# Performance work log

Hardware: AMD Instinct MI355X
Metric: run time of the kernel (lower is better)

The kernel has to match this reference:

```python
import jax, jax.numpy as jnp
import numpy as np

N_NODES = 50000
N_GRAPHS = 512
EPS = 1e-5


def _ln(x, g, b):
    mu = jnp.mean(x, axis=-1, keepdims=True)
    var = jnp.var(x, axis=-1, keepdims=True)
    return (x - mu) * jax.lax.rsqrt(var + EPS) * g + b


def _sage(x, src, dst, wl, wr, bl):
    # mean-aggregate neighbor features: messages x[src] -> dst
    s = jax.ops.segment_sum(x[src], dst, num_segments=N_NODES)
    cnt = jax.ops.segment_sum(jnp.ones((src.shape[0],), x.dtype), dst, num_segments=N_NODES)
    agg = s / jnp.maximum(cnt, 1.0)[:, None]
    # PyG SAGEConv: lin_l(agg) + lin_r(x), bias only on lin_l
    return agg @ wl + bl + x @ wr


def setup_inputs() -> dict:
    key = jax.random.key(0)
    ks = jax.random.split(key, 16)
    C, H, NC, E = 128, 128, 2, 800000
    inp = {
        'x': jax.random.normal(ks[0], (N_NODES, C), jnp.float32),
        'edge_index': jax.random.randint(ks[1], (2, E), 0, N_NODES, jnp.int32),
        'batch': jnp.sort(jax.random.randint(ks[2], (N_NODES,), 0, N_GRAPHS, jnp.int32)),
    }
    def w(k, shape):
        return jax.random.normal(k, shape, jnp.float32) * 0.05
    inp.update({
        'w1l': w(ks[3], (C, H)), 'w1r': w(ks[4], (C, H)), 'b1': jnp.zeros((H,), jnp.float32),
        'g1': jnp.ones((H,), jnp.float32), 'be1': jnp.zeros((H,), jnp.float32),
        'w2l': w(ks[5], (H, H)), 'w2r': w(ks[6], (H, H)), 'b2': jnp.zeros((H,), jnp.float32),
        'g2': jnp.ones((H,), jnp.float32), 'be2': jnp.zeros((H,), jnp.float32),
        'w3l': w(ks[7], (H, H)), 'w3r': w(ks[8], (H, H)), 'b3': jnp.zeros((H,), jnp.float32),
        'g3': jnp.ones((H,), jnp.float32), 'be3': jnp.zeros((H,), jnp.float32),
        'wc': w(ks[9], (H, NC)), 'bc': jnp.zeros((NC,), jnp.float32),
    })
    return inp


def reference(x, edge_index, batch, w1l, w1r, b1, g1, be1, w2l, w2r, b2, g2, be2,
              w3l, w3r, b3, g3, be3, wc, bc):
    src, dst = edge_index[0], edge_index[1]
    # eval mode: dropout is identity
    h1 = _ln(jax.nn.relu(_sage(x, src, dst, w1l, w1r, b1)), g1, be1)
    h2 = _ln(jax.nn.relu(_sage(h1, src, dst, w2l, w2r, b2)) + h1, g2, be2)
    h3 = _ln(h2 + jax.nn.relu(_sage(h2, src, dst, w3l, w3r, b3)), g3, be3)
    # global mean pool over graphs
    s = jax.ops.segment_sum(h3, batch, num_segments=N_GRAPHS)
    cnt = jax.ops.segment_sum(jnp.ones((h3.shape[0],), h3.dtype), batch, num_segments=N_GRAPHS)
    avg = s / jnp.maximum(cnt, 1.0)[:, None]
    out = avg @ wc + bc
    return (out, h3, avg)
```

## Files before the change

kernel.cpp:

```cpp
#include <hip/hip_runtime.h>

#define NND 50000
#define NE  800000
#define CF  128
#define NGR 512
#define DCAP 64

typedef __bf16 bf16;
typedef __bf16 bf16x2 __attribute__((ext_vector_type(2)));
typedef __bf16 bf16x4 __attribute__((ext_vector_type(4)));
typedef __bf16 bf16x8 __attribute__((ext_vector_type(8)));
typedef float  f32x4  __attribute__((ext_vector_type(4)));

__device__ __forceinline__ int swz(int n, int k) {
  return n * 256 + (((k >> 3) ^ (n & 31)) << 3) + (k & 7);
}

__global__ __launch_bounds__(256) void conv_k(const float* __restrict__ x,
                                              bf16* __restrict__ xb,
                                              const float* __restrict__ w1l, const float* __restrict__ w1r,
                                              const float* __restrict__ w2l, const float* __restrict__ w2r,
                                              const float* __restrict__ w3l, const float* __restrict__ w3r,
                                              bf16* __restrict__ wb,
                                              const int* __restrict__ batch,
                                              int* __restrict__ gs,
                                              int* __restrict__ cnt) {
  int t = blockIdx.x * 256 + threadIdx.x;
  if (t < (NND * CF / 4)) {
    f32x4 v = ((const f32x4*)x)[t];
    bf16x4 o;
    o[0] = (bf16)v[0]; o[1] = (bf16)v[1]; o[2] = (bf16)v[2]; o[3] = (bf16)v[3];
    ((bf16x4*)xb)[t] = o;
  }
  if (t < 49152) {
    int m = t >> 13, w = t & 8191;
    const float* src = (m == 0) ? w1l : (m == 1) ? w1r : (m == 2) ? w2l
                     : (m == 3) ? w2r : (m == 4) ? w3l : w3r;
    float2 v = *(const float2*)(src + w * 2);
    bf16x2 o;
    o[0] = (bf16)v.x; o[1] = (bf16)v.y;
    ((bf16x2*)wb)[t] = o;
  }
  if (t < NND) {
    cnt[t] = 0;
    int b = batch[t];
    if (t == 0) {
      for (int g = 0; g <= b; g++) gs[g] = 0;
    } else {
      int pb = batch[t - 1];
      for (int g = pb + 1; g <= b; g++) gs[g] = t;
    }
    if (t == NND - 1) {
      for (int g = b + 1; g <= NGR; g++) gs[g] = NND;
    }
  }
}

__global__ __launch_bounds__(256) void fill_k(const int* __restrict__ src,
                                              const int* __restrict__ dst,
                                              int* __restrict__ cnt,
                                              unsigned short* __restrict__ csr) {
  int r  = blockIdx.x & 7;
  int lo = r * 6250, hi = lo + 6250;
  int base = (blockIdx.x >> 3) * 2048;
  int end  = min(base + 2048, NE);
  for (int e = base + threadIdx.x; e < end; e += 256) {
    int d = dst[e];
    if (d >= lo && d < hi) {
      int p = atomicAdd(&cnt[d], 1);
      if (p < DCAP) csr[d * DCAP + p] = (unsigned short)src[e];
    }
  }
}

__global__ __launch_bounds__(256) void agg_k(const bf16* __restrict__ xin,
                                             const int* __restrict__ cnt,
                                             const unsigned short* __restrict__ csr,
                                             bf16* __restrict__ aggout) {
  int wid  = (blockIdx.x * 256 + threadIdx.x) >> 6;
  int lane = threadIdx.x & 63;
  if (wid >= NND) return;
  int sub = lane >> 4;
  int c8  = (lane & 15) * 8;
  int deg = min(cnt[wid], DCAP);
  int ebase = wid * DCAP;
  float a[8] = {};
  for (int e = 0; e < deg; e += 16) {
    int   s[4];
    float m[4];
#pragma unroll
    for (int u = 0; u < 4; u++) {
      int i = e + u * 4 + sub;
      s[u] = csr[ebase + ((i < deg) ? i : 0)];
      m[u] = (i < deg) ? 1.f : 0.f;
    }
    bf16x8 v[4];
#pragma unroll
    for (int u = 0; u < 4; u++) v[u] = *(const bf16x8*)(xin + s[u] * 128 + c8);
#pragma unroll
    for (int u = 0; u < 4; u++)
#pragma unroll
      for (int j = 0; j < 8; j++) a[j] += m[u] * (float)v[u][j];
  }
#pragma unroll
  for (int j = 0; j < 8; j++) {
    a[j] += __shfl_xor(a[j], 16);
    a[j] += __shfl_xor(a[j], 32);
  }
  if (sub == 0) {
    float inv = 1.0f / fmaxf((float)deg, 1.0f);
    bf16x8 o;
#pragma unroll
    for (int j = 0; j < 8; j++) o[j] = (bf16)(a[j] * inv);
    *(bf16x8*)(aggout + wid * 128 + c8) = o;
  }
}

template <typename TO>
__global__ __launch_bounds__(256, 2) void gemm_k(
    const bf16* __restrict__ aggp, const bf16* __restrict__ prev,
    const bf16* __restrict__ wl, const bf16* __restrict__ wr,
    const float* __restrict__ bias, const float* __restrict__ gamma,
    const float* __restrict__ beta, TO* __restrict__ outp, int addres) {
  __shared__ bf16 bt[128 * 256];
  int tid = threadIdx.x;
  for (int e = tid; e < 128 * 64; e += 256) {
    int k  = e >> 6;
    int n2 = (e & 63) << 1;
    {
      bf16x2 v = *(const bf16x2*)(wl + k * 128 + n2);
      bt[swz(n2, k)]     = v[0];
      bt[swz(n2 + 1, k)] = v[1];
    }
    {
      bf16x2 v = *(const bf16x2*)(wr + k * 128 + n2);
      bt[swz(n2, k + 128)]     = v[0];
      bt[swz(n2 + 1, k + 128)] = v[1];
    }
  }
  __syncthreads();

  int wave = tid >> 6, lane = tid & 63;
  int q = lane >> 4, r = lane & 15;
  int wrow = blockIdx.x * 128 + wave * 32;

  int arow[2];
#pragma unroll
  for (int rt = 0; rt < 2; rt++) {
    int ar = wrow + rt * 16 + r;
    arow[rt] = (ar < NND) ? ar : (NND - 1);
  }

  f32x4 acc[2][8] = {};

#pragma unroll
  for (int kk = 0; kk < 8; kk++) {
    int kof = kk * 32 + q * 8;
    bf16x8 af[2];
#pragma unroll
    for (int rt = 0; rt < 2; rt++) {
      const bf16* ap = (kk < 4) ? (aggp + arow[rt] * 128 + kof)
                                : (prev + arow[rt] * 128 + (kof - 128));
      af[rt] = *(const bf16x8*)ap;
    }
#pragma unroll
    for (int t = 0; t < 8; t++) {
      int n = t * 16 + r;
      bf16x8 bfrag = *(const bf16x8*)&bt[n * 256 + (((kof >> 3) ^ (n & 31)) << 3)];
#pragma unroll
      for (int rt = 0; rt < 2; rt++)
        acc[rt][t] = __builtin_amdgcn_mfma_f32_16x16x32_bf16(af[rt], bfrag, acc[rt][t], 0, 0, 0);
    }
  }

  float biasf[8], gf[8], bef[8];
#pragma unroll
  for (int t = 0; t < 8; t++) {
    int c = t * 16 + r;
    biasf[t] = bias[c];
    gf[t]    = gamma[c];
    bef[t]   = beta[c];
  }

#pragma unroll
  for (int rt = 0; rt < 2; rt++) {
#pragma unroll
    for (int reg = 0; reg < 4; reg++) {
      int row = wrow + rt * 16 + q * 4 + reg;
      int rr  = (row < NND) ? row : (NND - 1);
      const bf16* prow = prev + rr * 128;
      float vals[8];
      float s = 0.f, s2 = 0.f;
#pragma unroll
      for (int t = 0; t < 8; t++) {
        float v = acc[rt][t][reg] + biasf[t];
        v = fmaxf(v, 0.f);
        if (addres) v += (float)prow[t * 16 + r];
        vals[t] = v;
        s += v;
        s2 += v * v;
      }
#pragma unroll
      for (int m = 1; m < 16; m <<= 1) {
        s  += __shfl_xor(s, m);
        s2 += __shfl_xor(s2, m);
      }
      float mean = s * (1.f / 128.f);
      float var  = fmaxf(s2 * (1.f / 128.f) - mean * mean, 0.f);
      float rstd = rsqrtf(var + 1e-5f);
      if (row < NND) {
        TO* orow = outp + row * 128;
#pragma unroll
        for (int t = 0; t < 8; t++)
          orow[t * 16 + r] = (TO)((vals[t] - mean) * rstd * gf[t] + bef[t]);
      }
    }
  }
}

__global__ __launch_bounds__(256) void poolhead_k(
    const float* __restrict__ h3, const int* __restrict__ gs,
    const float* __restrict__ wc, const float* __restrict__ bc,
    float* __restrict__ outv, float* __restrict__ avgv) {
  int g = blockIdx.x;
  int s = gs[g], epos = gs[g + 1];
  int tid = threadIdx.x;
  int wave = tid >> 6, lane = tid & 63;
  float a0 = 0.f, a1 = 0.f;
  for (int row = s + wave; row < epos; row += 4) {
    float2 v = *(const float2*)(h3 + row * 128 + 2 * lane);
    a0 += v.x; a1 += v.y;
  }
  __shared__ float red[4][128];
  red[wave][2 * lane]     = a0;
  red[wave][2 * lane + 1] = a1;
  __syncthreads();
  __shared__ float sp[4];
  if (tid < 128) {
    float t4  = red[0][tid] + red[1][tid] + red[2][tid] + red[3][tid];
    float inv = 1.f / fmaxf((float)(epos - s), 1.f);
    float avg = t4 * inv;
    avgv[g * 128 + tid] = avg;
    float p0 = avg * wc[tid * 2 + 0];
    float p1 = avg * wc[tid * 2 + 1];
#pragma unroll
    for (int m = 1; m < 64; m <<= 1) {
      p0 += __shfl_xor(p0, m);
      p1 += __shfl_xor(p1, m);
    }
    if ((tid & 63) == 0) {
      sp[(tid >> 6) * 2]     = p0;
      sp[(tid >> 6) * 2 + 1] = p1;
    }
  }
  __syncthreads();
  if (tid == 0) {
    outv[g * 2 + 0] = sp[0] + sp[2] + bc[0];
    outv[g * 2 + 1] = sp[1] + sp[3] + bc[1];
  }
}

extern "C" void kernel_launch(void* const* d_in, const int* in_sizes, int n_in,
                              void* d_out, int out_size, void* d_ws, size_t ws_size,
                              hipStream_t stream) {
  const float* x   = (const float*)d_in[0];
  const int* ei    = (const int*)d_in[1];
  const int* batch = (const int*)d_in[2];
  const float* w1l = (const float*)d_in[3],  *w1r = (const float*)d_in[4];
  const float* b1  = (const float*)d_in[5],  *g1  = (const float*)d_in[6],  *be1 = (const float*)d_in[7];
  const float* w2l = (const float*)d_in[8],  *w2r = (const float*)d_in[9];
  const float* b2  = (const float*)d_in[10], *g2  = (const float*)d_in[11], *be2 = (const float*)d_in[12];
  const float* w3l = (const float*)d_in[13], *w3r = (const float*)d_in[14];
  const float* b3  = (const float*)d_in[15], *g3  = (const float*)d_in[16], *be3 = (const float*)d_in[17];
  const float* wc  = (const float*)d_in[18], *bc  = (const float*)d_in[19];
  const int* srcv = ei;
  const int* dstv = ei + NE;

  char* base = (char*)d_ws;
  int*            cnt  = (int*)(base + 0);
  int*            gs   = (int*)(base + 200064);
  bf16*           wb   = (bf16*)(base + 202752);
  unsigned short* csr  = (unsigned short*)(base + 399360);
  bf16*           agg  = (bf16*)(base + 6799360);
  bf16*           h1   = (bf16*)(base + 19599360);
  bf16*           h2xb = (bf16*)(base + 32399360);

  bf16* wb1l = wb,          *wb1r = wb + 16384;
  bf16* wb2l = wb + 32768,  *wb2r = wb + 49152;
  bf16* wb3l = wb + 65536,  *wb3r = wb + 81920;

  float* outv = (float*)d_out;
  float* h3   = outv + 1024;
  float* avgv = outv + 1024 + NND * CF;

  conv_k<<<6250, 256, 0, stream>>>(x, h2xb, w1l, w1r, w2l, w2r, w3l, w3r, wb, batch, gs, cnt);
  fill_k<<<3128, 256, 0, stream>>>(srcv, dstv, cnt, csr);

  agg_k<<<12500, 256, 0, stream>>>(h2xb, cnt, csr, agg);
  gemm_k<bf16><<<391, 256, 0, stream>>>(agg, h2xb, wb1l, wb1r, b1, g1, be1, h1, 0);
  agg_k<<<12500, 256, 0, stream>>>(h1, cnt, csr, agg);
  gemm_k<bf16><<<391, 256, 0, stream>>>(agg, h1, wb2l, wb2r, b2, g2, be2, h2xb, 1);
  agg_k<<<12500, 256, 0, stream>>>(h2xb, cnt, csr, agg);
  gemm_k<float><<<391, 256, 0, stream>>>(agg, h2xb, wb3l, wb3r, b3, g3, be3, h3, 1);
  poolhead_k<<<NGR, 256, 0, stream>>>(h3, gs, wc, bc, outv, avgv);
}
```

Measured before the change: 315.4 us.

## Fuse neighbor mean aggregation into the SAGE GEMM kernel

Removes the separate aggregation kernel and its intermediate buffer. Each GEMM wave now gathers and averages its own rows' neighbor features from the CSR into registers, then feeds them straight into the MFMA A-fragments. This saves three kernel launches and the write and re-read of the aggregated activations. The cost is that the irregular gather now runs with far fewer threads (391 blocks instead of 12500), with each lane looping serially over the neighbors, so latency hiding may suffer.

```diff
diff --git a/kernel.cpp b/kernel.cpp
--- a/kernel.cpp
+++ b/kernel.cpp
@@ -73,52 +73,10 @@
   }
 }
 
-__global__ __launch_bounds__(256) void agg_k(const bf16* __restrict__ xin,
-                                             const int* __restrict__ cnt,
-                                             const unsigned short* __restrict__ csr,
-                                             bf16* __restrict__ aggout) {
-  int wid  = (blockIdx.x * 256 + threadIdx.x) >> 6;
-  int lane = threadIdx.x & 63;
-  if (wid >= NND) return;
-  int sub = lane >> 4;
-  int c8  = (lane & 15) * 8;
-  int deg = min(cnt[wid], DCAP);
-  int ebase = wid * DCAP;
-  float a[8] = {};
-  for (int e = 0; e < deg; e += 16) {
-    int   s[4];
-    float m[4];
-#pragma unroll
-    for (int u = 0; u < 4; u++) {
-      int i = e + u * 4 + sub;
-      s[u] = csr[ebase + ((i < deg) ? i : 0)];
-      m[u] = (i < deg) ? 1.f : 0.f;
-    }
-    bf16x8 v[4];
-#pragma unroll
-    for (int u = 0; u < 4; u++) v[u] = *(const bf16x8*)(xin + s[u] * 128 + c8);
-#pragma unroll
-    for (int u = 0; u < 4; u++)
-#pragma unroll
-      for (int j = 0; j < 8; j++) a[j] += m[u] * (float)v[u][j];
-  }
-#pragma unroll
-  for (int j = 0; j < 8; j++) {
-    a[j] += __shfl_xor(a[j], 16);
-    a[j] += __shfl_xor(a[j], 32);
-  }
-  if (sub == 0) {
-    float inv = 1.0f / fmaxf((float)deg, 1.0f);
-    bf16x8 o;
-#pragma unroll
-    for (int j = 0; j < 8; j++) o[j] = (bf16)(a[j] * inv);
-    *(bf16x8*)(aggout + wid * 128 + c8) = o;
-  }
-}
-
 template <typename TO>
-__global__ __launch_bounds__(256, 2) void gemm_k(
-    const bf16* __restrict__ aggp, const bf16* __restrict__ prev,
+__global__ __launch_bounds__(256, 2) void aggemm_k(
+    const bf16* __restrict__ xp,
+    const int* __restrict__ cnt, const unsigned short* __restrict__ csr,
     const bf16* __restrict__ wl, const bf16* __restrict__ wr,
     const float* __restrict__ bias, const float* __restrict__ gamma,
     const float* __restrict__ beta, TO* __restrict__ outp, int addres) {
@@ -151,17 +109,63 @@
     arow[rt] = (ar < NND) ? ar : (NND - 1);
   }
 
+  bf16x8 aggf[2][4];
+#pragma unroll
+  for (int rt = 0; rt < 2; rt++) {
+    int row = arow[rt];
+    int deg = min(cnt[row], DCAP);
+    const unsigned short* cp = csr + row * DCAP;
+    const bf16* xq = xp + q * 8;
+    float fa[4][8] = {};
+    int e = 0;
+    for (; e + 2 <= deg; e += 2) {
+      ushort2 ss = *(const ushort2*)(cp + e);
+      const bf16* p0 = xq + (int)ss.x * 128;
+      const bf16* p1 = xq + (int)ss.y * 128;
+      bf16x8 v0[4], v1[4];
+#pragma unroll
+      for (int kk = 0; kk < 4; kk++) {
+        v0[kk] = *(const bf16x8*)(p0 + kk * 32);
+        v1[kk] = *(const bf16x8*)(p1 + kk * 32);
+      }
+#pragma unroll
+      for (int kk = 0; kk < 4; kk++)
+#pragma unroll
+        for (int j = 0; j < 8; j++)
+          fa[kk][j] += (float)v0[kk][j] + (float)v1[kk][j];
+    }
+    if (e < deg) {
+      const bf16* p0 = xq + (int)cp[e] * 128;
+#pragma unroll
+      for (int kk = 0; kk < 4; kk++) {
+        bf16x8 vt = *(const bf16x8*)(p0 + kk * 32);
+#pragma unroll
+        for (int j = 0; j < 8; j++) fa[kk][j] += (float)vt[j];
+      }
+    }
+    float inv = 1.0f / fmaxf((float)deg, 1.0f);
+#pragma unroll
+    for (int kk = 0; kk < 4; kk++) {
+      bf16x8 o;
+#pragma unroll
+      for (int j = 0; j < 8; j++) o[j] = (bf16)(fa[kk][j] * inv);
+      aggf[rt][kk] = o;
+    }
+  }
+
   f32x4 acc[2][8] = {};
 
 #pragma unroll
   for (int kk = 0; kk < 8; kk++) {
     int kof = kk * 32 + q * 8;
     bf16x8 af[2];
-#pragma unroll
-    for (int rt = 0; rt < 2; rt++) {
-      const bf16* ap = (kk < 4) ? (aggp + arow[rt] * 128 + kof)
-                                : (prev + arow[rt] * 128 + (kof - 128));
-      af[rt] = *(const bf16x8*)ap;
+    if (kk < 4) {
+      af[0] = aggf[0][kk];
+      af[1] = aggf[1][kk];
+    } else {
+#pragma unroll
+      for (int rt = 0; rt < 2; rt++)
+        af[rt] = *(const bf16x8*)(xp + arow[rt] * 128 + (kof - 128));
     }
 #pragma unroll
     for (int t = 0; t < 8; t++) {
@@ -188,7 +192,7 @@
     for (int reg = 0; reg < 4; reg++) {
       int row = wrow + rt * 16 + q * 4 + reg;
       int rr  = (row < NND) ? row : (NND - 1);
-      const bf16* prow = prev + rr * 128;
+      const bf16* prow = xp + rr * 128;
       float vals[8];
       float s = 0.f, s2 = 0.f;
 #pragma unroll
@@ -281,7 +285,6 @@
   int*            gs   = (int*)(base + 200064);
   bf16*           wb   = (bf16*)(base + 202752);
   unsigned short* csr  = (unsigned short*)(base + 399360);
-  bf16*           agg  = (bf16*)(base + 6799360);
   bf16*           h1   = (bf16*)(base + 19599360);
   bf16*           h2xb = (bf16*)(base + 32399360);
 
@@ -296,11 +299,8 @@
   conv_k<<<6250, 256, 0, stream>>>(x, h2xb, w1l, w1r, w2l, w2r, w3l, w3r, wb, batch, gs, cnt);
   fill_k<<<3128, 256, 0, stream>>>(srcv, dstv, cnt, csr);
 
-  agg_k<<<12500, 256, 0, stream>>>(h2xb, cnt, csr, agg);
-  gemm_k<bf16><<<391, 256, 0, stream>>>(agg, h2xb, wb1l, wb1r, b1, g1, be1, h1, 0);
-  agg_k<<<12500, 256, 0, stream>>>(h1, cnt, csr, agg);
-  gemm_k<bf16><<<391, 256, 0, stream>>>(agg, h1, wb2l, wb2r, b2, g2, be2, h2xb, 1);
-  agg_k<<<12500, 256, 0, stream>>>(h2xb, cnt, csr, agg);
-  gemm_k<float><<<391, 256, 0, stream>>>(agg, h2xb, wb3l, wb3r, b3, g3, be3, h3, 1);
+  aggemm_k<bf16><<<391, 256, 0, stream>>>(h2xb, cnt, csr, wb1l, wb1r, b1, g1, be1, h1, 0);
+  aggemm_k<bf16><<<391, 256, 0, stream>>>(h1, cnt, csr, wb2l, wb2r, b2, g2, be2, h2xb, 1);
+  aggemm_k<float><<<391, 256, 0, stream>>>(h2xb, cnt, csr, wb3l, wb3r, b3, g3, be3, h3, 1);
   poolhead_k<<<NGR, 256, 0, stream>>>(h3, gs, wc, bc, outv, avgv);
 }
```

After: 349.9 us. 10.9% more time.

## Split aggregation across four column quarters and simplify CSR fill

Applied to the files above, without the earlier changes.

The edge-fill kernel drops its 8-way destination-range partitioning, in which each block rescanned its edge chunk and kept only one eighth of the destinations. Each thread now loads four edges with int4 loads and inserts all of them, so each edge is read once. The aggregation kernel now gives each wavefront one node and one 32-column quarter, with 16 edges gathered in parallel at 16 bytes per lane. That raises the grid to 50000 blocks and adds two extra shuffle steps. The trade is more parallelism and shorter per-wave gather chains against four times the CSR index reads and a less localised atomic pattern in the fill.

```diff
diff --git a/kernel.cpp b/kernel.cpp
--- a/kernel.cpp
+++ b/kernel.cpp
@@ -60,16 +60,17 @@
                                               const int* __restrict__ dst,
                                               int* __restrict__ cnt,
                                               unsigned short* __restrict__ csr) {
-  int r  = blockIdx.x & 7;
-  int lo = r * 6250, hi = lo + 6250;
-  int base = (blockIdx.x >> 3) * 2048;
-  int end  = min(base + 2048, NE);
-  for (int e = base + threadIdx.x; e < end; e += 256) {
-    int d = dst[e];
-    if (d >= lo && d < hi) {
-      int p = atomicAdd(&cnt[d], 1);
-      if (p < DCAP) csr[d * DCAP + p] = (unsigned short)src[e];
-    }
+  int e = blockIdx.x * 1024 + threadIdx.x * 4;
+  if (e >= NE) return;
+  int4 d4 = *(const int4*)(dst + e);
+  int4 s4 = *(const int4*)(src + e);
+  int dd[4] = {d4.x, d4.y, d4.z, d4.w};
+  int ss[4] = {s4.x, s4.y, s4.z, s4.w};
+#pragma unroll
+  for (int u = 0; u < 4; u++) {
+    int d = dd[u];
+    int p = atomicAdd(&cnt[d], 1);
+    if (p < DCAP) csr[d * DCAP + p] = (unsigned short)ss[u];
   }
 }
 
@@ -77,42 +78,57 @@
                                              const int* __restrict__ cnt,
                                              const unsigned short* __restrict__ csr,
                                              bf16* __restrict__ aggout) {
-  int wid  = (blockIdx.x * 256 + threadIdx.x) >> 6;
+  int b = blockIdx.x;
+  int q = b & 3;
+  int node = (b >> 2) * 4 + (threadIdx.x >> 6);
   int lane = threadIdx.x & 63;
-  if (wid >= NND) return;
-  int sub = lane >> 4;
-  int c8  = (lane & 15) * 8;
-  int deg = min(cnt[wid], DCAP);
-  int ebase = wid * DCAP;
+  int esub = lane >> 2;
+  int coff = q * 32 + (lane & 3) * 8;
+  int deg = min(cnt[node], DCAP);
+  int ebase = node * DCAP;
   float a[8] = {};
-  for (int e = 0; e < deg; e += 16) {
-    int   s[4];
-    float m[4];
-#pragma unroll
-    for (int u = 0; u < 4; u++) {
-      int i = e + u * 4 + sub;
-      s[u] = csr[ebase + ((i < deg) ? i : 0)];
-      m[u] = (i < deg) ? 1.f : 0.f;
-    }
-    bf16x8 v[4];
-#pragma unroll
-    for (int u = 0; u < 4; u++) v[u] = *(const bf16x8*)(xin + s[u] * 128 + c8);
-#pragma unroll
-    for (int u = 0; u < 4; u++)
-#pragma unroll
-      for (int j = 0; j < 8; j++) a[j] += m[u] * (float)v[u][j];
+  {
+    int s[2]; float m[2]; bf16x8 v[2];
+    {
+      int i = esub;
+      s[0] = csr[ebase + ((i < deg) ? i : 0)];
+      m[0] = (i < deg) ? 1.f : 0.f;
+      v[0] = *(const bf16x8*)(xin + s[0] * 128 + coff);
+    }
+    if (deg > 16) {
+      int i = 16 + esub;
+      s[1] = csr[ebase + ((i < deg) ? i : 0)];
+      m[1] = (i < deg) ? 1.f : 0.f;
+      v[1] = *(const bf16x8*)(xin + s[1] * 128 + coff);
+    }
+#pragma unroll
+    for (int j = 0; j < 8; j++) a[j] += m[0] * (float)v[0][j];
+    if (deg > 16) {
+#pragma unroll
+      for (int j = 0; j < 8; j++) a[j] += m[1] * (float)v[1][j];
+    }
+  }
+  for (int e0 = 32; e0 < deg; e0 += 16) {
+    int i = e0 + esub;
+    int s = csr[ebase + ((i < deg) ? i : 0)];
+    float m = (i < deg) ? 1.f : 0.f;
+    bf16x8 v = *(const bf16x8*)(xin + s * 128 + coff);
+#pragma unroll
+    for (int j = 0; j < 8; j++) a[j] += m * (float)v[j];
   }
 #pragma unroll
   for (int j = 0; j < 8; j++) {
+    a[j] += __shfl_xor(a[j], 4);
+    a[j] += __shfl_xor(a[j], 8);
     a[j] += __shfl_xor(a[j], 16);
     a[j] += __shfl_xor(a[j], 32);
   }
-  if (sub == 0) {
+  if (esub == 0) {
     float inv = 1.0f / fmaxf((float)deg, 1.0f);
     bf16x8 o;
 #pragma unroll
     for (int j = 0; j < 8; j++) o[j] = (bf16)(a[j] * inv);
-    *(bf16x8*)(aggout + wid * 128 + c8) = o;
+    *(bf16x8*)(aggout + node * 128 + coff) = o;
   }
 }
 
@@ -294,13 +310,13 @@
   float* avgv = outv + 1024 + NND * CF;
 
   conv_k<<<6250, 256, 0, stream>>>(x, h2xb, w1l, w1r, w2l, w2r, w3l, w3r, wb, batch, gs, cnt);
-  fill_k<<<3128, 256, 0, stream>>>(srcv, dstv, cnt, csr);
-
-  agg_k<<<12500, 256, 0, stream>>>(h2xb, cnt, csr, agg);
+  fill_k<<<782, 256, 0, stream>>>(srcv, dstv, cnt, csr);
+
+  agg_k<<<50000, 256, 0, stream>>>(h2xb, cnt, csr, agg);
   gemm_k<bf16><<<391, 256, 0, stream>>>(agg, h2xb, wb1l, wb1r, b1, g1, be1, h1, 0);
-  agg_k<<<12500, 256, 0, stream>>>(h1, cnt, csr, agg);
+  agg_k<<<50000, 256, 0, stream>>>(h1, cnt, csr, agg);
   gemm_k<bf16><<<391, 256, 0, stream>>>(agg, h1, wb2l, wb2r, b2, g2, be2, h2xb, 1);
-  agg_k<<<12500, 256, 0, stream>>>(h2xb, cnt, csr, agg);
+  agg_k<<<50000, 256, 0, stream>>>(h2xb, cnt, csr, agg);
   gemm_k<float><<<391, 256, 0, stream>>>(agg, h2xb, wb3l, wb3r, b3, g3, be3, h3, 1);
   poolhead_k<<<NGR, 256, 0, stream>>>(h3, gs, wc, bc, outv, avgv);
 }
```

Result: slower. 453.0 us (+43.6%).
